# Performance work log

Measured on AMD Instinct MI355X. Metric: run time of the kernel, lower is better.

Reference implementation:

```python
import jax, jax.numpy as jnp
import numpy as np

B, F, S, D, DL = 8, 4096, 1024, 128, 256  # batch, facts/batch, seq_len, d_model, d_latent
N_PRED = 14
LN_EPS = 1e-5


def setup_inputs() -> dict:
    key = jax.random.key(0)
    ks = jax.random.split(key, 16)
    return {
        "a0": jax.random.randint(ks[0], (B, F), 0, S),
        "a1": jax.random.randint(ks[1], (B, F), 0, S),
        "pred_idx": jax.random.randint(ks[2], (B, F), 0, 13),
        "bidir": jax.random.randint(ks[3], (B, F), 0, 2).astype(jnp.float32),
        "pos_emb": jax.random.normal(ks[4], (S, D), jnp.float32) * 0.02,
        "pred_emb": jax.random.normal(ks[5], (N_PRED, D), jnp.float32) * 0.02,
        "w1": jax.random.normal(ks[6], (3 * D, 2 * D), jnp.float32) / np.sqrt(3 * D),
        "b1": jnp.zeros((2 * D,), jnp.float32),
        "w2": jax.random.normal(ks[7], (2 * D, D), jnp.float32) / np.sqrt(2 * D),
        "b2": jnp.zeros((D,), jnp.float32),
        "ln_g": jnp.ones((D,), jnp.float32),
        "ln_b": jnp.zeros((D,), jnp.float32),
        "lw1": jax.random.normal(ks[8], (D, DL), jnp.float32) / np.sqrt(D),
        "lb1": jnp.zeros((DL,), jnp.float32),
        "lw2": jax.random.normal(ks[9], (DL, DL), jnp.float32) / np.sqrt(DL),
        "lb2": jnp.zeros((DL,), jnp.float32),
    }


def reference(a0, a1, pred_idx, bidir, pos_emb, pred_emb,
              w1, b1, w2, b2, ln_g, ln_b, lw1, lb1, lw2, lb2):
    nodes = pos_emb  # [S, D] shared base node features (pos embedding)

    def msg_mlp(x):  # [..., 3D] -> [..., D], exact (erf) GELU like torch default
        return jax.nn.gelu(x @ w1 + b1, approximate=False) @ w2 + b2

    na0 = nodes[a0]          # [B, F, D]
    na1 = nodes[a1]          # [B, F, D]
    pe = pred_emb[pred_idx]  # [B, F, D]

    msg01 = msg_mlp(jnp.concatenate([na0, pe, na1], axis=-1))  # added at a1
    msg10 = msg_mlp(jnp.concatenate([na1, pe, na0], axis=-1))  # added at a0 if bidir

    # flatten batch into segment offsets for one big scatter-add
    off = (jnp.arange(B, dtype=a0.dtype) * S)[:, None]
    agg = jnp.zeros((B * S, D), msg01.dtype)
    agg = agg.at[(a1 + off).reshape(-1)].add(msg01.reshape(-1, D))
    agg = agg.at[(a0 + off).reshape(-1)].add((msg10 * bidir[..., None]).reshape(-1, D))
    agg = agg.reshape(B, S, D)

    h = nodes[None, :, :] + agg  # [B, S, D]
    mu = jnp.mean(h, axis=-1, keepdims=True)
    var = jnp.mean(jnp.square(h - mu), axis=-1, keepdims=True)
    h = (h - mu) * jax.lax.rsqrt(var + LN_EPS) * ln_g + ln_b

    pooled = jnp.mean(h, axis=1)  # [B, D]
    latent = jax.nn.gelu(pooled @ lw1 + lb1, approximate=False) @ lw2 + lb2
    return latent  # [B, DL]
```

## Files before the change

kernel.cpp:

```cpp
#include <hip/hip_runtime.h>
#include <hip/hip_bf16.h>

#define BB 8
#define FF 4096
#define SS 1024
#define DD 128
#define DLL 256
#define NF (BB*FF)
#define NMSG (2*NF)
#define NNODE (BB*SS)
#define CAP 36

typedef short  short8 __attribute__((ext_vector_type(8)));
typedef float  f32x4  __attribute__((ext_vector_type(4)));

__device__ __forceinline__ uint f2bf(float x) {
    uint u = __float_as_uint(x);
    return (u + 0x7fffu + ((u >> 16) & 1u)) >> 16;
}
__device__ __forceinline__ float bf2f(uint lo16) {
    return __uint_as_float(lo16 << 16);
}

__device__ __forceinline__ float gelu_fast(float x) {
    const float z = fabsf(x) * 0.70710678118654752440f;
    const float t = __builtin_amdgcn_rcpf(__builtin_fmaf(0.3275911f, z, 1.0f));
    float p = 1.061405429f;
    p = __builtin_fmaf(p, t, -1.453152027f);
    p = __builtin_fmaf(p, t, 1.421413741f);
    p = __builtin_fmaf(p, t, -0.284496736f);
    p = __builtin_fmaf(p, t, 0.254829592f);
    p *= t;
    const float e = __expf(-z * z);
    const float erfv = __builtin_fmaf(-p, e, 1.0f);
    return 0.5f * x * (1.0f + copysignf(erfv, x));
}

__global__ __launch_bounds__(256) void zero_kernel(int* __restrict__ cnt,
                                                   float* __restrict__ pooled)
{
    const int i = blockIdx.x * 256 + threadIdx.x;
    if (i < NNODE) { cnt[i] = 0; return; }
    const int j = i - NNODE;
    if (j < BB * DD) pooled[j] = 0.0f;
}

#define N_W2 (256*128)
#define PA_BLOCKS 256
#define PE0       PA_BLOCKS
#define FLAT0     (PA_BLOCKS + 4)
#define N_FLAT    (N_W2 + NMSG)
#define FLAT_BLOCKS ((N_FLAT + 255) / 256)
#define PREP_GRID (FLAT0 + FLAT_BLOCKS)

__global__ __launch_bounds__(256) void prep_kernel(
    const float* __restrict__ pos_emb, const float* __restrict__ pred_emb,
    const float* __restrict__ w1, const float* __restrict__ b1,
    const float* __restrict__ w2,
    const int* __restrict__ a0, const int* __restrict__ a1,
    const int* __restrict__ pidx, const float* __restrict__ bidir,
    ushort* __restrict__ Pa, ushort* __restrict__ Pc, ushort* __restrict__ PE,
    ushort* __restrict__ w2p, int* __restrict__ cnt, uint* __restrict__ idx32)
{
    const int blk = blockIdx.x;
    const int tid = threadIdx.x;

    if (blk < PA_BLOCKS) {
        __shared__ float ps[4][128];
        const int s0 = blk * 4;
        for (int q = tid; q < 512; q += 256) ps[q >> 7][q & 127] = pos_emb[s0 * 128 + q];
        __syncthreads();
        const int j = tid;
        float aa[4], ac[4];
        #pragma unroll
        for (int r = 0; r < 4; ++r) { aa[r] = 0.0f; ac[r] = 0.0f; }
        #pragma unroll 4
        for (int k = 0; k < 128; ++k) {
            const float wa = w1[k * 256 + j];
            const float wc = w1[(256 + k) * 256 + j];
            #pragma unroll
            for (int r = 0; r < 4; ++r) {
                aa[r] = __builtin_fmaf(ps[r][k], wa, aa[r]);
                ac[r] = __builtin_fmaf(ps[r][k], wc, ac[r]);
            }
        }
        #pragma unroll
        for (int r = 0; r < 4; ++r) {
            Pa[(s0 + r) * 256 + j] = (ushort)f2bf(aa[r]);
            Pc[(s0 + r) * 256 + j] = (ushort)f2bf(ac[r]);
        }
        return;
    }
    if (blk < FLAT0) {
        __shared__ float w1s[128][64];
        __shared__ float prs[16][128];
        const int j0 = (blk - PE0) * 64;
        for (int q = tid; q < 128 * 64; q += 256) {
            const int k = q >> 6, jj = q & 63;
            w1s[k][jj] = w1[(128 + k) * 256 + j0 + jj];
        }
        for (int q = tid; q < 16 * 128; q += 256)
            prs[q >> 7][q & 127] = (q < 14 * 128) ? pred_emb[q] : 0.0f;
        __syncthreads();
        const int jl = tid & 63, rq = tid >> 6;
        float acc[4] = {0.0f, 0.0f, 0.0f, 0.0f};
        #pragma unroll 8
        for (int k = 0; k < 128; ++k) {
            const float wv = w1s[k][jl];
            #pragma unroll
            for (int i = 0; i < 4; ++i)
                acc[i] = __builtin_fmaf(prs[rq + 4 * i][k], wv, acc[i]);
        }
        const float bj = b1[j0 + jl];
        #pragma unroll
        for (int i = 0; i < 4; ++i) {
            const int r = rq + 4 * i;
            if (r < 14) PE[r * 256 + j0 + jl] = (ushort)f2bf(acc[i] + bj);
        }
        return;
    }
    int i = (blk - FLAT0) * 256 + tid;
    if (i < N_W2) {
        const int k = i >> 7, d = i & 127;
        const int d0 = d >> 4, lr = d & 15, ks = k >> 5, lq = (k >> 3) & 3, e = k & 7;
        w2p[(d0 * 8 + ks) * 512 + lr * 32 + lq * 8 + e] = (ushort)f2bf(w2[i]);
        return;
    }
    i -= N_W2;
    if (i < NMSG) {
        const int g = i >> 1, p = i & 1;
        const float w = p ? bidir[g] : 1.0f;
        if (w != 0.0f) {
            const int ra0 = a0[g], ra1 = a1[g];
            const int X = p ? ra1 : ra0;
            const int Y = p ? ra0 : ra1;
            const int dest = p ? ra0 : ra1;
            const int nid = ((g >> 12) << 10) + dest;
            const int slot = atomicAdd(&cnt[nid], 1);
            if (slot < CAP)
                idx32[nid * CAP + slot] = (uint)X | ((uint)Y << 10) | ((uint)pidx[g] << 20);
        }
    }
}

__global__ __launch_bounds__(512, 2) void node_kernel(
    const ushort* __restrict__ Pa, const ushort* __restrict__ Pc,
    const ushort* __restrict__ PE,
    const ushort* __restrict__ w2p, const float* __restrict__ b2,
    const float* __restrict__ pos_emb,
    const int* __restrict__ cnt, const uint* __restrict__ idx32,
    const float* __restrict__ ln_g, const float* __restrict__ ln_b,
    float* __restrict__ pooled)
{
    __shared__ uint4 h1g[512];
    __shared__ float wsumS[16];
    __shared__ float aggf[16][132];
    __shared__ float red[8][128];

    const int tid = threadIdx.x;
    const int wid = tid >> 6, lane = tid & 63;
    const int lq = lane >> 4, lr = lane & 15;
    const int nbase = blockIdx.x * 16;

    #pragma unroll
    for (int i = 0; i < 2; ++i) {
        const int n = wid * 2 + i;
        const int nid = nbase + n;
        int c = cnt[nid]; if (c > CAP) c = CAP;
        const uint* bucket = idx32 + nid * CAP;
        float G0 = 0.0f, G1 = 0.0f, G2 = 0.0f, G3 = 0.0f;
        for (int j = 0; j < c; ++j) {
            const uint e = bucket[j];
            const int X = e & 1023;
            const int Y = (e >> 10) & 1023;
            const int rpi = e >> 20;
            const uint2 ua = *(const uint2*)(Pa + X * 256 + lane * 4);
            const uint2 ub = *(const uint2*)(PE + rpi * 256 + lane * 4);
            const uint2 uc = *(const uint2*)(Pc + Y * 256 + lane * 4);
            const float h0 = bf2f(ua.x & 0xffffu) + bf2f(ub.x & 0xffffu) + bf2f(uc.x & 0xffffu);
            const float h1 = bf2f(ua.x >> 16)     + bf2f(ub.x >> 16)     + bf2f(uc.x >> 16);
            const float h2 = bf2f(ua.y & 0xffffu) + bf2f(ub.y & 0xffffu) + bf2f(uc.y & 0xffffu);
            const float h3 = bf2f(ua.y >> 16)     + bf2f(ub.y >> 16)     + bf2f(uc.y >> 16);
            G0 += gelu_fast(h0);
            G1 += gelu_fast(h1);
            G2 += gelu_fast(h2);
            G3 += gelu_fast(h3);
        }
        uint2 t;
        t.x = f2bf(G0) | (f2bf(G1) << 16);
        t.y = f2bf(G2) | (f2bf(G3) << 16);
        const int col = lane * 8;
        const int byteoff = n * 512 + ((((col >> 4)) ^ (n & 15)) << 4) + (col & 15);
        *(uint2*)((char*)h1g + byteoff) = t;
        if (lane == 0) wsumS[n] = (float)c;
    }
    __syncthreads();

    f32x4 acc = (f32x4)0.0f;
    #pragma unroll
    for (int ks = 0; ks < 8; ++ks) {
        const int m = lr;
        const short8 hfrag = *(const short8*)((char*)h1g + m * 512 + ((((ks * 4 + lq)) ^ (m & 15)) << 4));
        const short8 wfrag = *(const short8*)(w2p + (wid * 8 + ks) * 512 + lr * 32 + lq * 8);
        acc = __builtin_amdgcn_mfma_f32_16x16x32_bf16(wfrag, hfrag, acc, 0, 0, 0);
    }

    {
        const float wsm = wsumS[lr];
        const int s = (nbase + lr) & (SS - 1);
        const int d0 = wid * 16 + lq * 4;
        const float4 b24 = *(const float4*)(b2 + d0);
        const float4 pe4 = *(const float4*)(pos_emb + s * DD + d0);
        float4 o;
        o.x = __builtin_fmaf(wsm, b24.x, acc[0] + pe4.x);
        o.y = __builtin_fmaf(wsm, b24.y, acc[1] + pe4.y);
        o.z = __builtin_fmaf(wsm, b24.z, acc[2] + pe4.z);
        o.w = __builtin_fmaf(wsm, b24.w, acc[3] + pe4.w);
        *(float4*)&aggf[lr][d0] = o;
    }
    __syncthreads();

    const float g0 = ln_g[lane], g1 = ln_g[lane + 64];
    const float bb0 = ln_b[lane], bb1 = ln_b[lane + 64];
    float p0 = 0.0f, p1 = 0.0f;
    #pragma unroll
    for (int i = 0; i < 2; ++i) {
        const int n = wid * 2 + i;
        const float h0 = aggf[n][lane];
        const float h1 = aggf[n][lane + 64];
        float sum = h0 + h1;
        #pragma unroll
        for (int o = 32; o > 0; o >>= 1) sum += __shfl_xor(sum, o);
        const float mu = sum * (1.0f / 128.0f);
        const float d0 = h0 - mu, d1 = h1 - mu;
        float sq = d0 * d0 + d1 * d1;
        #pragma unroll
        for (int o = 32; o > 0; o >>= 1) sq += __shfl_xor(sq, o);
        const float rstd = rsqrtf(sq * (1.0f / 128.0f) + 1e-5f);
        p0 += d0 * rstd * g0 + bb0;
        p1 += d1 * rstd * g1 + bb1;
    }
    red[wid][lane]      = p0;
    red[wid][lane + 64] = p1;
    __syncthreads();
    if (tid < 128) {
        float v = 0.0f;
        #pragma unroll
        for (int w = 0; w < 8; ++w) v += red[w][tid];
        const int b = nbase >> 10;
        atomicAdd(&pooled[b * DD + tid], v);
    }
}

__global__ __launch_bounds__(256) void head_kernel(
    const float* __restrict__ pooled,
    const float* __restrict__ lw1, const float* __restrict__ lb1,
    const float* __restrict__ lw2, const float* __restrict__ lb2,
    float* __restrict__ out)
{
    const int b = blockIdx.x;
    const int j = threadIdx.x;
    __shared__ float p[128];
    __shared__ float t1[256];
    if (j < 128) p[j] = pooled[b*DD + j] * (1.0f / (float)SS);
    __syncthreads();
    float acc = lb1[j];
    #pragma unroll 8
    for (int k = 0; k < 128; ++k) acc = __builtin_fmaf(p[k], lw1[k * 256 + j], acc);
    t1[j] = gelu_fast(acc);
    __syncthreads();
    float acc2 = lb2[j];
    #pragma unroll 8
    for (int k = 0; k < 256; ++k) acc2 = __builtin_fmaf(t1[k], lw2[k * 256 + j], acc2);
    out[b*DLL + j] = acc2;
}

extern "C" void kernel_launch(void* const* d_in, const int* in_sizes, int n_in,
                              void* d_out, int out_size, void* d_ws, size_t ws_size,
                              hipStream_t stream) {
    const int*   a0       = (const int*)d_in[0];
    const int*   a1       = (const int*)d_in[1];
    const int*   pidx     = (const int*)d_in[2];
    const float* bidir    = (const float*)d_in[3];
    const float* pos_emb  = (const float*)d_in[4];
    const float* pred_emb = (const float*)d_in[5];
    const float* w1       = (const float*)d_in[6];
    const float* b1       = (const float*)d_in[7];
    const float* w2       = (const float*)d_in[8];
    const float* b2       = (const float*)d_in[9];
    const float* ln_g     = (const float*)d_in[10];
    const float* ln_b     = (const float*)d_in[11];
    const float* lw1      = (const float*)d_in[12];
    const float* lb1      = (const float*)d_in[13];
    const float* lw2      = (const float*)d_in[14];
    const float* lb2      = (const float*)d_in[15];

    char* ws = (char*)d_ws;
    const size_t O_CNT  = 0;
    const size_t O_POOL = 32768;
    const size_t O_IDX  = O_POOL + 4096;
    const size_t O_W2P  = O_IDX + (size_t)NNODE * CAP * 4;
    const size_t O_PA   = O_W2P + 65536;
    const size_t O_PC   = O_PA + 524288;
    const size_t O_PE   = O_PC + 524288;

    int*    cnt    = (int*)(ws + O_CNT);
    float*  pooled = (float*)(ws + O_POOL);
    uint*   idx32  = (uint*)(ws + O_IDX);
    ushort* w2p    = (ushort*)(ws + O_W2P);
    ushort* Pa     = (ushort*)(ws + O_PA);
    ushort* Pc     = (ushort*)(ws + O_PC);
    ushort* PE     = (ushort*)(ws + O_PE);

    zero_kernel<<<(NNODE + BB*DD + 255) / 256, 256, 0, stream>>>(cnt, pooled);
    prep_kernel<<<PREP_GRID, 256, 0, stream>>>(
        pos_emb, pred_emb, w1, b1, w2, a0, a1, pidx, bidir,
        Pa, Pc, PE, w2p, cnt, idx32);
    node_kernel<<<NNODE / 16, 512, 0, stream>>>(
        Pa, Pc, PE, w2p, b2, pos_emb, cnt, idx32, ln_g, ln_b, pooled);
    head_kernel<<<BB, 256, 0, stream>>>(pooled, lw1, lb1, lw2, lb2, (float*)d_out);
}
```

Baseline: 49.34 us.

## Process one node per wave in node_kernel and prefetch next gather entry

Halves the nodes handled per block from 16 to 8, so each wave aggregates one node instead of two, and doubles the grid size. The gather loop is software-pipelined: the three bf16 rows for the next bucket entry are loaded before the GELU of the current one. Launch bounds now ask for 8 blocks of 512 threads per unit. The aim is to hide gather latency with more waves in flight and more overlapped loads. The cost is that half the MFMA tile now computes on unwritten shared-memory rows whose results are thrown away, and twice as many atomic adds go into pooled.

After: 46.85 us. 1.05x faster.

```diff
diff --git a/kernel.cpp b/kernel.cpp
--- a/kernel.cpp
+++ b/kernel.cpp
@@ -143,7 +143,7 @@
     }
 }
 
-__global__ __launch_bounds__(512, 2) void node_kernel(
+__global__ __launch_bounds__(512, 8) void node_kernel(
     const ushort* __restrict__ Pa, const ushort* __restrict__ Pc,
     const ushort* __restrict__ PE,
     const ushort* __restrict__ w2p, const float* __restrict__ b2,
@@ -153,46 +153,44 @@
     float* __restrict__ pooled)
 {
     __shared__ uint4 h1g[512];
-    __shared__ float wsumS[16];
-    __shared__ float aggf[16][132];
+    __shared__ float wsumS[8];
+    __shared__ float aggf[8][132];
     __shared__ float red[8][128];
 
     const int tid = threadIdx.x;
     const int wid = tid >> 6, lane = tid & 63;
     const int lq = lane >> 4, lr = lane & 15;
-    const int nbase = blockIdx.x * 16;
-
-    #pragma unroll
-    for (int i = 0; i < 2; ++i) {
-        const int n = wid * 2 + i;
-        const int nid = nbase + n;
+    const int nbase = blockIdx.x * 8;
+
+    {
+        const int nid = nbase + wid;
         int c = cnt[nid]; if (c > CAP) c = CAP;
         const uint* bucket = idx32 + nid * CAP;
         float G0 = 0.0f, G1 = 0.0f, G2 = 0.0f, G3 = 0.0f;
-        for (int j = 0; j < c; ++j) {
-            const uint e = bucket[j];
-            const int X = e & 1023;
-            const int Y = (e >> 10) & 1023;
-            const int rpi = e >> 20;
-            const uint2 ua = *(const uint2*)(Pa + X * 256 + lane * 4);
-            const uint2 ub = *(const uint2*)(PE + rpi * 256 + lane * 4);
-            const uint2 uc = *(const uint2*)(Pc + Y * 256 + lane * 4);
-            const float h0 = bf2f(ua.x & 0xffffu) + bf2f(ub.x & 0xffffu) + bf2f(uc.x & 0xffffu);
-            const float h1 = bf2f(ua.x >> 16)     + bf2f(ub.x >> 16)     + bf2f(uc.x >> 16);
-            const float h2 = bf2f(ua.y & 0xffffu) + bf2f(ub.y & 0xffffu) + bf2f(uc.y & 0xffffu);
-            const float h3 = bf2f(ua.y >> 16)     + bf2f(ub.y >> 16)     + bf2f(uc.y >> 16);
-            G0 += gelu_fast(h0);
-            G1 += gelu_fast(h1);
-            G2 += gelu_fast(h2);
-            G3 += gelu_fast(h3);
+        if (c > 0) {
+            uint e = bucket[0];
+            uint2 ua = *(const uint2*)(Pa + (e & 1023) * 256 + lane * 4);
+            uint2 ub = *(const uint2*)(PE + (e >> 20) * 256 + lane * 4);
+            uint2 uc = *(const uint2*)(Pc + ((e >> 10) & 1023) * 256 + lane * 4);
+            for (int j = 0; j < c; ++j) {
+                const uint en = bucket[(j + 1 < c) ? j + 1 : j];
+                const uint2 ua_n = *(const uint2*)(Pa + (en & 1023) * 256 + lane * 4);
+                const uint2 ub_n = *(const uint2*)(PE + (en >> 20) * 256 + lane * 4);
+                const uint2 uc_n = *(const uint2*)(Pc + ((en >> 10) & 1023) * 256 + lane * 4);
+                G0 += gelu_fast(bf2f(ua.x & 0xffffu) + bf2f(ub.x & 0xffffu) + bf2f(uc.x & 0xffffu));
+                G1 += gelu_fast(bf2f(ua.x >> 16)     + bf2f(ub.x >> 16)     + bf2f(uc.x >> 16));
+                G2 += gelu_fast(bf2f(ua.y & 0xffffu) + bf2f(ub.y & 0xffffu) + bf2f(uc.y & 0xffffu));
+                G3 += gelu_fast(bf2f(ua.y >> 16)     + bf2f(ub.y >> 16)     + bf2f(uc.y >> 16));
+                ua = ua_n; ub = ub_n; uc = uc_n;
+            }
         }
         uint2 t;
         t.x = f2bf(G0) | (f2bf(G1) << 16);
         t.y = f2bf(G2) | (f2bf(G3) << 16);
         const int col = lane * 8;
-        const int byteoff = n * 512 + ((((col >> 4)) ^ (n & 15)) << 4) + (col & 15);
+        const int byteoff = wid * 512 + ((((col >> 4)) ^ (wid & 15)) << 4) + (col & 15);
         *(uint2*)((char*)h1g + byteoff) = t;
-        if (lane == 0) wsumS[n] = (float)c;
+        if (lane == 0) wsumS[wid] = (float)c;
     }
     __syncthreads();
 
@@ -205,7 +203,7 @@
         acc = __builtin_amdgcn_mfma_f32_16x16x32_bf16(wfrag, hfrag, acc, 0, 0, 0);
     }
 
-    {
+    if (lr < 8) {
         const float wsm = wsumS[lr];
         const int s = (nbase + lr) & (SS - 1);
         const int d0 = wid * 16 + lq * 4;
@@ -220,14 +218,11 @@
     }
     __syncthreads();
 
-    const float g0 = ln_g[lane], g1 = ln_g[lane + 64];
-    const float bb0 = ln_b[lane], bb1 = ln_b[lane + 64];
-    float p0 = 0.0f, p1 = 0.0f;
-    #pragma unroll
-    for (int i = 0; i < 2; ++i) {
-        const int n = wid * 2 + i;
-        const float h0 = aggf[n][lane];
-        const float h1 = aggf[n][lane + 64];
+    {
+        const float g0 = ln_g[lane], g1 = ln_g[lane + 64];
+        const float bb0 = ln_b[lane], bb1 = ln_b[lane + 64];
+        const float h0 = aggf[wid][lane];
+        const float h1 = aggf[wid][lane + 64];
         float sum = h0 + h1;
         #pragma unroll
         for (int o = 32; o > 0; o >>= 1) sum += __shfl_xor(sum, o);
@@ -237,11 +232,9 @@
         #pragma unroll
         for (int o = 32; o > 0; o >>= 1) sq += __shfl_xor(sq, o);
         const float rstd = rsqrtf(sq * (1.0f / 128.0f) + 1e-5f);
-        p0 += d0 * rstd * g0 + bb0;
-        p1 += d1 * rstd * g1 + bb1;
-    }
-    red[wid][lane]      = p0;
-    red[wid][lane + 64] = p1;
+        red[wid][lane]      = d0 * rstd * g0 + bb0;
+        red[wid][lane + 64] = d1 * rstd * g1 + bb1;
+    }
     __syncthreads();
     if (tid < 128) {
         float v = 0.0f;
@@ -316,7 +309,7 @@
     prep_kernel<<<PREP_GRID, 256, 0, stream>>>(
         pos_emb, pred_emb, w1, b1, w2, a0, a1, pidx, bidir,
         Pa, Pc, PE, w2p, cnt, idx32);
-    node_kernel<<<NNODE / 16, 512, 0, stream>>>(
+    node_kernel<<<NNODE / 8, 512, 0, stream>>>(
         Pa, Pc, PE, w2p, b2, pos_emb, cnt, idx32, ln_g, ln_b, pooled);
     head_kernel<<<BB, 256, 0, stream>>>(pooled, lw1, lb1, lw2, lb2, (float*)d_out);
 }
```
